# Optimization experiments

Measured on AMD Instinct MI355X. Metric: run time of the kernel, lower is better.

Reference implementation:

```python
import jax, jax.numpy as jnp
import numpy as np

E = 256
H = 8
DH = E // H
N = 200000
NEG = -1e9


def _normalize(x, eps=1e-12):
    # torch F.normalize: x / max(||x||_2, eps) along last dim
    n = jnp.linalg.norm(x, axis=-1, keepdims=True)
    return x / jnp.maximum(n, eps)


def setup_inputs() -> dict:
    key = jax.random.key(0)
    ks = jax.random.split(key, 16)
    s = 1.0 / np.sqrt(E)
    inp = {
        "context_vector": jax.random.normal(ks[0], (3 * E,), jnp.float32),
        "node_embeddings": jax.random.normal(ks[1], (N, E), jnp.float32),
        "invalid_action_mask": jax.random.randint(ks[2], (N,), 0, 2).astype(bool),
        # project_context: Linear(3E, E)
        "Wc": jax.random.normal(ks[3], (E, 3 * E), jnp.float32) * (1.0 / np.sqrt(3 * E)),
        "bc": jnp.zeros((E,), jnp.float32),
        # project_keys / project_values: Linear(E, E)
        "Wk": jax.random.normal(ks[4], (E, E), jnp.float32) * s,
        "bk": jnp.zeros((E,), jnp.float32),
        "Wv": jax.random.normal(ks[5], (E, E), jnp.float32) * s,
        "bv": jnp.zeros((E,), jnp.float32),
        # nn.MultiheadAttention packed in-projection and out-projection
        "in_proj_w": jax.random.normal(ks[6], (3 * E, E), jnp.float32) * s,
        "in_proj_b": jnp.zeros((3 * E,), jnp.float32),
        "out_proj_w": jax.random.normal(ks[7], (E, E), jnp.float32) * s,
        "out_proj_b": jnp.zeros((E,), jnp.float32),
        # project_attn_output: Linear(E, E)
        "Wo": jax.random.normal(ks[8], (E, E), jnp.float32) * s,
        "bo": jnp.zeros((E,), jnp.float32),
    }
    # guarantee at least one valid action
    inp["invalid_action_mask"] = inp["invalid_action_mask"].at[0].set(False)
    return inp


def reference(context_vector, node_embeddings, invalid_action_mask,
              Wc, bc, Wk, bk, Wv, bv,
              in_proj_w, in_proj_b, out_proj_w, out_proj_b, Wo, bo):
    valid = ~invalid_action_mask                        # [N]

    query = context_vector @ Wc.T + bc                  # [E]
    keys = _normalize(node_embeddings @ Wk.T + bk)      # [N, E]
    values = _normalize(node_embeddings @ Wv.T + bv)    # [N, E]

    # MultiheadAttention, single query, batch 1
    wq, wk2, wv2 = in_proj_w[:E], in_proj_w[E:2 * E], in_proj_w[2 * E:]
    bq, bk2, bv2 = in_proj_b[:E], in_proj_b[E:2 * E], in_proj_b[2 * E:]
    q = (query @ wq.T + bq).reshape(H, DH)              # [H, DH]
    k = (keys @ wk2.T + bk2).reshape(N, H, DH)          # [N, H, DH]
    v = (values @ wv2.T + bv2).reshape(N, H, DH)

    logits = jnp.einsum("hd,nhd->hn", q, k) / np.sqrt(DH)   # [H, N]
    logits = jnp.where(valid[None, :], logits, NEG)
    w = jax.nn.softmax(logits, axis=-1)                 # [H, N]
    attn = jnp.einsum("hn,nhd->hd", w, v).reshape(E)    # [E]
    attn = attn @ out_proj_w.T + out_proj_b             # [E]

    attn = _normalize(attn @ Wo.T + bo)                 # [E]

    # pointer scores over valid nodes (invalid -> prob 0)
    scores = jnp.where(valid, keys @ attn, NEG)         # [N]
    probs = jax.nn.softmax(scores)                      # [N]
    return probs
```

## Files before the change

kernel.cpp:

```cpp
#include <hip/hip_runtime.h>

#define NN 200000
#define NEGV -1000000000.0f

typedef __attribute__((ext_vector_type(8))) short bf16x8;
typedef __attribute__((ext_vector_type(4))) float f32x4;
typedef __attribute__((ext_vector_type(4))) unsigned int u32x4;

__device__ __forceinline__ float bf2f(unsigned short u){
  unsigned int x = ((unsigned int)u) << 16;
  return __builtin_bit_cast(float, x);
}
__device__ __forceinline__ unsigned short f2bf(float f){
  unsigned int x = __builtin_bit_cast(unsigned int, f);
  x += 0x7fffu + ((x >> 16) & 1u);
  return (unsigned short)(x >> 16);
}

static constexpr size_t OFF_RK     = 0;
static constexpr size_t OFF_RV     = 800256;
static constexpr size_t OFF_LOGITS = 1600512;
static constexpr size_t OFF_SCORES = 8000512;
static constexpr size_t OFF_QUERY  = 8800768;
static constexpr size_t OFF_Q2     = 8801792;
static constexpr size_t OFF_A2     = 8802816;
static constexpr size_t OFF_CONSTS = 8811008;
static constexpr size_t OFF_BIMG   = 8811264;
static constexpr size_t OFF_LSTAT  = 9081600;
static constexpr size_t OFF_MZ     = 9089792;
static constexpr size_t OFF_KATTN  = 9089856;
static constexpr size_t OFF_KB     = 9090880;
static constexpr size_t OFF_UPART  = 9090944;
static constexpr size_t OFF_TPART  = 13285248;
static constexpr size_t OFF_U      = 13301632;
static constexpr size_t OFF_T      = 13309824;
static constexpr size_t OFF_P3STAT = 13309888;
static constexpr size_t OFF_MZ3    = 13313984;
static constexpr size_t OFF_EMBBF  = 13314048;
static constexpr size_t WS_NEED_BF = OFF_EMBBF + (size_t)NN*512;

__global__ void k_prep1(const float* __restrict__ ctx, const float* __restrict__ Wc,
                        const float* __restrict__ bc, float* __restrict__ query){
  int tid = threadIdx.x, lane = tid & 63, wave = tid >> 6;
  float4 c0 = *(const float4*)(ctx + lane*4);
  float4 c1 = *(const float4*)(ctx + 256 + lane*4);
  float4 c2 = *(const float4*)(ctx + 512 + lane*4);
  #pragma unroll
  for (int rr = 0; rr < 2; rr++){
    int r = blockIdx.x*8 + wave*2 + rr;
    float4 w0 = *(const float4*)(Wc + (size_t)r*768 + lane*4);
    float4 w1 = *(const float4*)(Wc + (size_t)r*768 + 256 + lane*4);
    float4 w2 = *(const float4*)(Wc + (size_t)r*768 + 512 + lane*4);
    float d = w0.x*c0.x + w0.y*c0.y + w0.z*c0.z + w0.w*c0.w
            + w1.x*c1.x + w1.y*c1.y + w1.z*c1.z + w1.w*c1.w
            + w2.x*c2.x + w2.y*c2.y + w2.z*c2.z + w2.w*c2.w;
    #pragma unroll
    for (int m = 1; m < 64; m <<= 1) d += __shfl_xor(d, m);
    if (lane == 0) query[r] = d + bc[r];
  }
}

__global__ void k_prep2(const float* __restrict__ ipw, const float* __restrict__ ipb,
                        const float* __restrict__ query, float* __restrict__ q2){
  int tid = threadIdx.x, lane = tid & 63, wave = tid >> 6;
  float4 x4 = *(const float4*)(query + lane*4);
  #pragma unroll
  for (int rr = 0; rr < 2; rr++){
    int r = blockIdx.x*8 + wave*2 + rr;
    float4 w4 = *(const float4*)(ipw + (size_t)r*256 + lane*4);
    float d = w4.x*x4.x + w4.y*x4.y + w4.z*x4.z + w4.w*x4.w;
    #pragma unroll
    for (int m = 1; m < 64; m <<= 1) d += __shfl_xor(d, m);
    if (lane == 0) q2[r] = d + ipb[r];
  }
}

__global__ void k_prep3(const float* __restrict__ ipw, const float* __restrict__ ipb,
                        const float* __restrict__ q2, float* __restrict__ AH,
                        float* __restrict__ consts){
  int h = blockIdx.x, t = threadIdx.x;
  __shared__ float qs[32];
  if (t < 32) qs[t] = q2[h*32 + t];
  __syncthreads();
  float a = 0.f;
  #pragma unroll
  for (int d = 0; d < 32; d++) a += qs[d] * ipw[(size_t)(256 + h*32 + d)*256 + t];
  AH[h*256 + t] = a;
  if (t == 0){
    float ck = 0.f;
    for (int d = 0; d < 32; d++) ck += qs[d] * ipb[256 + h*32 + d];
    consts[8 + h] = ck;
  }
}

__global__ void k_prep4(const float* __restrict__ Wk, const float* __restrict__ AH,
                        float* __restrict__ A2p){
  int b = blockIdx.x, h = b >> 3, seg = b & 7, t = threadIdx.x;
  __shared__ float as[32];
  if (t < 32) as[t] = AH[h*256 + seg*32 + t];
  __syncthreads();
  float acc = 0.f;
  #pragma unroll
  for (int i = 0; i < 32; i++) acc += as[i] * Wk[(size_t)(seg*32 + i)*256 + t];
  A2p[(size_t)b*256 + t] = acc;
}

__global__ void k_prep5(const float* __restrict__ A2p, const float* __restrict__ AH,
                        const float* __restrict__ bk, float* __restrict__ A2,
                        float* __restrict__ consts){
  int h = blockIdx.x, t = threadIdx.x, lane = t & 63, wave = t >> 6;
  float s = 0.f;
  #pragma unroll
  for (int seg = 0; seg < 8; seg++) s += A2p[(size_t)(h*8 + seg)*256 + t];
  A2[h*256 + t] = s;
  float cc = AH[h*256 + t] * bk[t];
  #pragma unroll
  for (int m = 1; m < 64; m <<= 1) cc += __shfl_xor(cc, m);
  __shared__ float red[4];
  if (lane == 0) red[wave] = cc;
  __syncthreads();
  if (t == 0) consts[h] = red[0] + red[1] + red[2] + red[3];
}

__global__ void k_bimg(const float* __restrict__ Wk, const float* __restrict__ Wv,
                       const float* __restrict__ A2, unsigned char* __restrict__ bimg){
  int g = blockIdx.x*256 + threadIdx.x;
  if (g >= 8*528*4) return;
  int s = g / (528*4);
  int rem = g % (528*4);
  int col = rem >> 2, kg = rem & 3;
  int j0 = s*32 + kg*8;
  const float* src = nullptr;
  if (col < 256) src = Wk + col*256 + j0;
  else if (col < 512) src = Wv + (col-256)*256 + j0;
  else if (col < 520) src = A2 + (col-512)*256 + j0;
  unsigned short u[8];
  #pragma unroll
  for (int i = 0; i < 8; i++) u[i] = src ? f2bf(src[i]) : (unsigned short)0;
  uint4 o;
  o.x = (unsigned int)u[0] | ((unsigned int)u[1] << 16);
  o.y = (unsigned int)u[2] | ((unsigned int)u[3] << 16);
  o.z = (unsigned int)u[4] | ((unsigned int)u[5] << 16);
  o.w = (unsigned int)u[6] | ((unsigned int)u[7] << 16);
  unsigned int addr = (unsigned int)((col*64 + kg*16) ^ ((col & 7) << 4));
  *(uint4*)(bimg + (size_t)s*33792 + addr) = o;
}

__launch_bounds__(512)
__global__ void k_main(const float* __restrict__ emb, const unsigned char* __restrict__ bimg,
                       const int* __restrict__ mask, const float* __restrict__ consts,
                       float* __restrict__ rk_g, float* __restrict__ rv_g,
                       float* __restrict__ logits, unsigned char* __restrict__ ebf){
  __shared__ float part[4][4][16];
  __shared__ float rkbuf[64];
  const int tid = threadIdx.x;
  const int lane = tid & 63, wave = tid >> 6;
  const int sp = wave >> 2, ch = wave & 3;
  const int c = lane & 15, kg = lane >> 4;
  const int nb0 = blockIdx.x * 64;
  const unsigned bOff = (unsigned)((c*64 + kg*16) ^ ((c & 7) << 4));
  const int node0 = (sp*2 + 0)*16 + c;
  const int node1 = (sp*2 + 1)*16 + c;
  const bool wr = (ch == 0) && (ebf != nullptr);

  f32x4 acc[2][9];
  #pragma unroll
  for (int st = 0; st < 2; st++)
    #pragma unroll
    for (int f = 0; f < 9; f++) acc[st][f] = (f32x4){0.f, 0.f, 0.f, 0.f};

  #pragma unroll 2
  for (int s = 0; s < 8; s++){
    const float* a0p = emb + (size_t)(nb0 + node0)*256 + s*32 + kg*8;
    const float* a1p = emb + (size_t)(nb0 + node1)*256 + s*32 + kg*8;
    float4 x0 = *(const float4*)a0p, x1 = *(const float4*)(a0p + 4);
    float4 y0 = *(const float4*)a1p, y1 = *(const float4*)(a1p + 4);
    u32x4 u0, u1;
    u0.x = (unsigned int)f2bf(x0.x) | ((unsigned int)f2bf(x0.y) << 16);
    u0.y = (unsigned int)f2bf(x0.z) | ((unsigned int)f2bf(x0.w) << 16);
    u0.z = (unsigned int)f2bf(x1.x) | ((unsigned int)f2bf(x1.y) << 16);
    u0.w = (unsigned int)f2bf(x1.z) | ((unsigned int)f2bf(x1.w) << 16);
    u1.x = (unsigned int)f2bf(y0.x) | ((unsigned int)f2bf(y0.y) << 16);
    u1.y = (unsigned int)f2bf(y0.z) | ((unsigned int)f2bf(y0.w) << 16);
    u1.z = (unsigned int)f2bf(y1.x) | ((unsigned int)f2bf(y1.y) << 16);
    u1.w = (unsigned int)f2bf(y1.z) | ((unsigned int)f2bf(y1.w) << 16);
    bf16x8 af0 = __builtin_bit_cast(bf16x8, u0);
    bf16x8 af1 = __builtin_bit_cast(bf16x8, u1);
    if (wr){
      unsigned char* base = ebf + (size_t)blockIdx.x*32768 + (size_t)s*4096;
      __builtin_nontemporal_store(u0, (u32x4*)(base + node0*64 + kg*16));
      __builtin_nontemporal_store(u1, (u32x4*)(base + node1*64 + kg*16));
    }
    const unsigned char* bs = bimg + (size_t)s*33792;
    #pragma unroll
    for (int f = 0; f < 9; f++){
      int cf = (f < 8) ? (ch*8 + f) : 32;
      bf16x8 bfv = *(const bf16x8*)(bs + (size_t)cf*1024 + bOff);
      acc[0][f] = __builtin_amdgcn_mfma_f32_16x16x32_bf16(af0, bfv, acc[0][f], 0, 0, 0);
      acc[1][f] = __builtin_amdgcn_mfma_f32_16x16x32_bf16(af1, bfv, acc[1][f], 0, 0, 0);
    }
  }

  #pragma unroll
  for (int st = 0; st < 2; st++){
    #pragma unroll
    for (int i = 0; i < 4; i++){
      float pp = 0.f;
      #pragma unroll
      for (int f = 0; f < 8; f++) pp += acc[st][f][i]*acc[st][f][i];
      #pragma unroll
      for (int m = 1; m < 16; m <<= 1) pp += __shfl_xor(pp, m);
      if (c == 0) part[ch][2*sp + st][kg*4 + i] = pp;
    }
  }
  __syncthreads();
  if (tid < 64){
    int gs = tid >> 4, r = tid & 15;
    float rk = fmaxf(sqrtf(part[0][gs][r] + part[1][gs][r]), 1e-12f);
    float rv = fmaxf(sqrtf(part[2][gs][r] + part[3][gs][r]), 1e-12f);
    rk_g[nb0 + tid] = rk; rv_g[nb0 + tid] = rv;
    rkbuf[tid] = rk;
  }
  __syncthreads();
  if (ch == 3 && c < 8){
    const float rs32 = 0.17677669529663688f;
    float cb = consts[c], ck = consts[8 + c];
    #pragma unroll
    for (int st = 0; st < 2; st++){
      #pragma unroll
      for (int i = 0; i < 4; i++){
        int nl = (2*sp + st)*16 + kg*4 + i;
        int n = nb0 + nl;
        float lg = (mask[n] == 0) ? ((acc[st][8][i] + cb)*rs32/rkbuf[nl] + ck*rs32) : NEGV;
        logits[(size_t)n*8 + c] = lg;
      }
    }
  }
}

__global__ void k_lstats(const float* __restrict__ logits, float* __restrict__ lstat){
  int tid = threadIdx.x;
  float m[8], z[8];
  #pragma unroll
  for (int h = 0; h < 8; h++){ m[h] = -3.0e38f; z[h] = 0.f; }
  for (int n = blockIdx.x*256 + tid; n < NN; n += 128*256){
    float4 a = *(const float4*)(logits + (size_t)n*8);
    float4 b = *(const float4*)(logits + (size_t)n*8 + 4);
    float l[8] = {a.x,a.y,a.z,a.w,b.x,b.y,b.z,b.w};
    #pragma unroll
    for (int h = 0; h < 8; h++){
      float M = fmaxf(m[h], l[h]);
      z[h] = z[h]*expf(m[h]-M) + expf(l[h]-M);
      m[h] = M;
    }
  }
  #pragma unroll
  for (int s = 1; s < 64; s <<= 1){
    #pragma unroll
    for (int h = 0; h < 8; h++){
      float m2 = __shfl_xor(m[h], s), z2 = __shfl_xor(z[h], s);
      float M = fmaxf(m[h], m2);
      z[h] = z[h]*expf(m[h]-M) + z2*expf(m2-M);
      m[h] = M;
    }
  }
  __shared__ float sm[4][8], sz[4][8];
  int wave = tid >> 6, lane = tid & 63;
  if (lane == 0){
    #pragma unroll
    for (int h = 0; h < 8; h++){ sm[wave][h] = m[h]; sz[wave][h] = z[h]; }
  }
  __syncthreads();
  if (tid < 8){
    float M = sm[0][tid], Z = sz[0][tid];
    #pragma unroll
    for (int w = 1; w < 4; w++){
      float M2 = fmaxf(M, sm[w][tid]);
      Z = Z*expf(M-M2) + sz[w][tid]*expf(sm[w][tid]-M2);
      M = M2;
    }
    lstat[(blockIdx.x*8 + tid)*2] = M;
    lstat[(blockIdx.x*8 + tid)*2 + 1] = Z;
  }
}

__global__ void k_mz(const float* __restrict__ lstat, float* __restrict__ MZ){
  int t = threadIdx.x;
  int h = t >> 3, seg = t & 7;
  float m = -3.0e38f, z = 0.f;
  for (int k = 0; k < 16; k++){
    int b = seg*16 + k;
    float m2 = lstat[(b*8 + h)*2], z2 = lstat[(b*8 + h)*2 + 1];
    float M = fmaxf(m, m2); z = z*expf(m-M) + z2*expf(m2-M); m = M;
  }
  #pragma unroll
  for (int s = 1; s < 8; s <<= 1){
    float m2 = __shfl_xor(m, s), z2 = __shfl_xor(z, s);
    float M = fmaxf(m, m2); z = z*expf(m-M) + z2*expf(m2-M); m = M;
  }
  if (seg == 0){ MZ[h] = m; MZ[8+h] = z; }
}

template<int BF>
__launch_bounds__(256)
__global__ void k_wsum(const void* __restrict__ embsrc, const float* __restrict__ logits,
                       const float* __restrict__ rv_g, const float* __restrict__ MZ,
                       float* __restrict__ upart, float* __restrict__ tpart){
  int tid = threadIdx.x, lane = tid & 63, wave = tid >> 6;
  int hl = lane & 31, h2 = lane >> 5;
  int gw = blockIdx.x*4 + wave;
  float Mh = MZ[hl & 7];
  float ua[8][8];
  #pragma unroll
  for (int h = 0; h < 8; h++)
    #pragma unroll
    for (int j = 0; j < 8; j++) ua[h][j] = 0.f;
  float tacc = 0.f;
  for (int p = gw; p < NN/2; p += 2048){
    int n = 2*p + h2;
    float e[8];
    if (BF){
      size_t addr = (size_t)(n >> 6)*32768 + (size_t)(hl >> 2)*4096
                  + (size_t)(n & 63)*64 + (size_t)(hl & 3)*16;
      uint4 g = *(const uint4*)((const unsigned char*)embsrc + addr);
      e[0]=bf2f((unsigned short)(g.x&0xffff)); e[1]=bf2f((unsigned short)(g.x>>16));
      e[2]=bf2f((unsigned short)(g.y&0xffff)); e[3]=bf2f((unsigned short)(g.y>>16));
      e[4]=bf2f((unsigned short)(g.z&0xffff)); e[5]=bf2f((unsigned short)(g.z>>16));
      e[6]=bf2f((unsigned short)(g.w&0xffff)); e[7]=bf2f((unsigned short)(g.w>>16));
    } else {
      const float* ep = (const float*)embsrc + (size_t)n*256 + hl*8;
      float4 a = *(const float4*)ep, b = *(const float4*)(ep + 4);
      e[0]=a.x; e[1]=a.y; e[2]=a.z; e[3]=a.w; e[4]=b.x; e[5]=b.y; e[6]=b.z; e[7]=b.w;
    }
    float coef = 0.f;
    if (hl < 8) coef = expf(logits[(size_t)n*8 + hl] - Mh) / rv_g[n];
    tacc += coef;
    #pragma unroll
    for (int h = 0; h < 8; h++){
      float ch = __shfl(coef, h, 32);
      #pragma unroll
      for (int j = 0; j < 8; j++) ua[h][j] += ch * e[j];
    }
  }
  #pragma unroll
  for (int h = 0; h < 8; h++)
    #pragma unroll
    for (int j = 0; j < 8; j++) ua[h][j] += __shfl_xor(ua[h][j], 32);
  tacc += __shfl_xor(tacc, 32);
  __shared__ float ub[4][8][256];
  __shared__ float tb[4][8];
  if (h2 == 0){
    #pragma unroll
    for (int h = 0; h < 8; h++)
      #pragma unroll
      for (int j = 0; j < 8; j++) ub[wave][h][hl*8 + j] = ua[h][j];
    if (hl < 8) tb[wave][hl] = tacc;
  }
  __syncthreads();
  #pragma unroll
  for (int rep = 0; rep < 8; rep++){
    int idx = rep*256 + tid;
    int h = idx >> 8, j = idx & 255;
    upart[(size_t)blockIdx.x*2048 + h*256 + j] = ub[0][h][j]+ub[1][h][j]+ub[2][h][j]+ub[3][h][j];
  }
  if (tid < 8) tpart[blockIdx.x*8 + tid] = tb[0][tid]+tb[1][tid]+tb[2][tid]+tb[3][tid];
}

__global__ void k_ured(const float* __restrict__ upart, const float* __restrict__ tpart,
                       float* __restrict__ U, float* __restrict__ T){
  int b = blockIdx.x; int h = b >> 3, js = b & 7;
  int t = threadIdx.x; int j = js*32 + (t & 31); int br = t >> 5;
  float s = 0.f;
  for (int k = 0; k < 64; k++){
    int bb = k*8 + br;
    s += upart[(size_t)bb*2048 + h*256 + j];
  }
  __shared__ float sb[8][32];
  sb[br][t & 31] = s;
  __syncthreads();
  if (t < 32){
    float tot = 0.f;
    #pragma unroll
    for (int r = 0; r < 8; r++) tot += sb[r][t];
    U[h*256 + js*32 + t] = tot;
  }
  if (js == 0){
    float tp = 0.f;
    for (int i = t; i < 512; i += 256) tp += tpart[i*8 + h];
    #pragma unroll
    for (int m = 1; m < 64; m <<= 1) tp += __shfl_xor(tp, m);
    __shared__ float rr[4];
    if ((t & 63) == 0) rr[t >> 6] = tp;
    __syncthreads();
    if (t == 0) T[h] = rr[0]+rr[1]+rr[2]+rr[3];
  }
}

__global__ void k_att1(const float* __restrict__ U, const float* __restrict__ T,
                       const float* __restrict__ MZ, const float* __restrict__ Wv,
                       const float* __restrict__ bv, float* __restrict__ sh2g){
  int tid = threadIdx.x, lane = tid & 63, wave = tid >> 6;
  float4 uh[8];
  #pragma unroll
  for (int h = 0; h < 8; h++) uh[h] = *(const float4*)(U + h*256 + lane*4);
  #pragma unroll
  for (int rr = 0; rr < 2; rr++){
    int r = blockIdx.x*8 + wave*2 + rr;
    float4 w4 = *(const float4*)(Wv + (size_t)r*256 + lane*4);
    float acc[8];
    #pragma unroll
    for (int h = 0; h < 8; h++)
      acc[h] = w4.x*uh[h].x + w4.y*uh[h].y + w4.z*uh[h].z + w4.w*uh[h].w;
    #pragma unroll
    for (int m = 1; m < 64; m <<= 1)
      #pragma unroll
      for (int h = 0; h < 8; h++) acc[h] += __shfl_xor(acc[h], m);
    if (lane == 0){
      float bvr = bv[r];
      #pragma unroll
      for (int h = 0; h < 8; h++) sh2g[h*256 + r] = (acc[h] + bvr*T[h]) / MZ[8+h];
    }
  }
}

__global__ void k_att2(const float* __restrict__ ipw, const float* __restrict__ ipb,
                       const float* __restrict__ sh2g, float* __restrict__ a1g){
  int tid = threadIdx.x, lane = tid & 63, wave = tid >> 6;
  #pragma unroll
  for (int rr = 0; rr < 2; rr++){
    int r = blockIdx.x*8 + wave*2 + rr;
    int h = r >> 5;
    float4 x4 = *(const float4*)(sh2g + h*256 + lane*4);
    float4 w4 = *(const float4*)(ipw + (size_t)(512 + r)*256 + lane*4);
    float d = w4.x*x4.x + w4.y*x4.y + w4.z*x4.z + w4.w*x4.w;
    #pragma unroll
    for (int m = 1; m < 64; m <<= 1) d += __shfl_xor(d, m);
    if (lane == 0) a1g[r] = d + ipb[512 + r];
  }
}

__global__ void k_matvec(const float* __restrict__ W, const float* __restrict__ b,
                         const float* __restrict__ x, float* __restrict__ y){
  int tid = threadIdx.x, lane = tid & 63, wave = tid >> 6;
  float4 x4 = *(const float4*)(x + lane*4);
  #pragma unroll
  for (int rr = 0; rr < 2; rr++){
    int r = blockIdx.x*8 + wave*2 + rr;
    float4 w4 = *(const float4*)(W + (size_t)r*256 + lane*4);
    float d = w4.x*x4.x + w4.y*x4.y + w4.z*x4.z + w4.w*x4.w;
    #pragma unroll
    for (int m = 1; m < 64; m <<= 1) d += __shfl_xor(d, m);
    if (lane == 0) y[r] = d + b[r];
  }
}

__global__ void k_att5(const float* __restrict__ Wk, const float* __restrict__ o2g,
                       float* __restrict__ kp){
  int b = blockIdx.x, t = threadIdx.x;
  __shared__ float os[32];
  if (t < 32) os[t] = o2g[b*32 + t];
  __syncthreads();
  float acc = 0.f;
  #pragma unroll
  for (int i = 0; i < 32; i++) acc += os[i] * Wk[(size_t)(b*32 + i)*256 + t];
  kp[b*256 + t] = acc;
}

__global__ void k_fin(const float* __restrict__ o2g, const float* __restrict__ kp,
                      const float* __restrict__ bk, float* __restrict__ kattn,
                      float* __restrict__ kbout){
  int t = threadIdx.x, lane = t & 63, wave = t >> 6;
  __shared__ float red[4], red2[4];
  float o2v = o2g[t];
  float sq = o2v*o2v;
  #pragma unroll
  for (int m = 1; m < 64; m <<= 1) sq += __shfl_xor(sq, m);
  if (lane == 0) red[wave] = sq;
  float cb = o2v * bk[t];
  #pragma unroll
  for (int m = 1; m < 64; m <<= 1) cb += __shfl_xor(cb, m);
  if (lane == 0) red2[wave] = cb;
  __syncthreads();
  float nrm = fmaxf(sqrtf(red[0]+red[1]+red[2]+red[3]), 1e-12f);
  float s = 0.f;
  #pragma unroll
  for (int b = 0; b < 8; b++) s += kp[b*256 + t];
  kattn[t] = s / nrm;
  if (t == 0) kbout[0] = (red2[0]+red2[1]+red2[2]+red2[3]) / nrm;
}

template<int BF>
__launch_bounds__(256)
__global__ void k_scores(const void* __restrict__ embsrc, const float* __restrict__ rk_g,
                         const int* __restrict__ mask, const float* __restrict__ kattn,
                         const float* __restrict__ kbp, float* __restrict__ scores,
                         float* __restrict__ p3stat){
  int tid = threadIdx.x, lane = tid & 63, wave = tid >> 6;
  int hl = lane & 31, h2 = lane >> 5;
  __shared__ float ka[256];
  ka[tid] = kattn[tid];
  __syncthreads();
  float kb = kbp[0];
  float kv[8];
  #pragma unroll
  for (int j = 0; j < 8; j++) kv[j] = ka[hl*8 + j];
  int gw = blockIdx.x*4 + wave;
  float m = -3.0e38f, z = 0.f;
  for (int p = gw; p < NN/2; p += 2048){
    int n = 2*p + h2;
    float d;
    if (BF){
      size_t addr = (size_t)(n >> 6)*32768 + (size_t)(hl >> 2)*4096
                  + (size_t)(n & 63)*64 + (size_t)(hl & 3)*16;
      uint4 g = *(const uint4*)((const unsigned char*)embsrc + addr);
      d  = bf2f((unsigned short)(g.x&0xffff))*kv[0] + bf2f((unsigned short)(g.x>>16))*kv[1];
      d += bf2f((unsigned short)(g.y&0xffff))*kv[2] + bf2f((unsigned short)(g.y>>16))*kv[3];
      d += bf2f((unsigned short)(g.z&0xffff))*kv[4] + bf2f((unsigned short)(g.z>>16))*kv[5];
      d += bf2f((unsigned short)(g.w&0xffff))*kv[6] + bf2f((unsigned short)(g.w>>16))*kv[7];
    } else {
      const float* ep = (const float*)embsrc + (size_t)n*256 + hl*8;
      float4 a = *(const float4*)ep, b = *(const float4*)(ep + 4);
      d = a.x*kv[0]+a.y*kv[1]+a.z*kv[2]+a.w*kv[3]+b.x*kv[4]+b.y*kv[5]+b.z*kv[6]+b.w*kv[7];
    }
    #pragma unroll
    for (int s = 1; s < 32; s <<= 1) d += __shfl_xor(d, s);
    if (hl == 0){
      float sc = (mask[n] == 0) ? ((d + kb) / rk_g[n]) : NEGV;
      scores[n] = sc;
      float M = fmaxf(m, sc);
      z = z*expf(m - M) + expf(sc - M);
      m = M;
    }
  }
  float m2 = __shfl_xor(m, 32), z2 = __shfl_xor(z, 32);
  float M = fmaxf(m, m2); z = z*expf(m-M) + z2*expf(m2-M); m = M;
  __shared__ float rm[4], rz[4];
  if (lane == 0){ rm[wave] = m; rz[wave] = z; }
  __syncthreads();
  if (tid == 0){
    float Mx = rm[0], Z = rz[0];
    for (int w = 1; w < 4; w++){
      float M2 = fmaxf(Mx, rm[w]);
      Z = Z*expf(Mx - M2) + rz[w]*expf(rm[w] - M2);
      Mx = M2;
    }
    p3stat[blockIdx.x*2] = Mx; p3stat[blockIdx.x*2+1] = Z;
  }
}

__global__ void k_mz3(const float* __restrict__ p3stat, float* __restrict__ MZ3){
  int t = threadIdx.x;
  float m = p3stat[t*2], z = p3stat[t*2+1];
  {
    float m2 = p3stat[(t+256)*2], z2 = p3stat[(t+256)*2+1];
    float M = fmaxf(m, m2); z = z*expf(m-M) + z2*expf(m2-M); m = M;
  }
  #pragma unroll
  for (int mm = 1; mm < 64; mm <<= 1){
    float ms = __shfl_xor(m, mm), zs = __shfl_xor(z, mm);
    float Mx = fmaxf(m, ms); z = z*expf(m-Mx) + zs*expf(ms-Mx); m = Mx;
  }
  __shared__ float rm[4], rz[4];
  if ((t&63)==0){ rm[t>>6]=m; rz[t>>6]=z; }
  __syncthreads();
  if (t==0){
    float M=rm[0], Z=rz[0];
    for (int w=1; w<4; w++){ float Mx=fmaxf(M,rm[w]); Z=Z*expf(M-Mx)+rz[w]*expf(rm[w]-Mx); M=Mx; }
    MZ3[0]=M; MZ3[1]=Z;
  }
}

__global__ void k_probs(const float* __restrict__ scores, const float* __restrict__ MZ3,
                        float* __restrict__ out){
  float M = MZ3[0], iZ = 1.0f / MZ3[1];
  for (int n = blockIdx.x*256 + threadIdx.x; n < NN; n += 512*256)
    out[n] = expf(scores[n] - M) * iZ;
}

extern "C" void kernel_launch(void* const* d_in, const int* in_sizes, int n_in,
                              void* d_out, int out_size, void* d_ws, size_t ws_size,
                              hipStream_t stream){
  (void)in_sizes; (void)n_in; (void)out_size;
  const float* ctx = (const float*)d_in[0];
  const float* emb = (const float*)d_in[1];
  const int*   mask= (const int*)d_in[2];
  const float* Wc  = (const float*)d_in[3];
  const float* bc  = (const float*)d_in[4];
  const float* Wk  = (const float*)d_in[5];
  const float* bk  = (const float*)d_in[6];
  const float* Wv  = (const float*)d_in[7];
  const float* bv  = (const float*)d_in[8];
  const float* ipw = (const float*)d_in[9];
  const float* ipb = (const float*)d_in[10];
  const float* opw = (const float*)d_in[11];
  const float* opb = (const float*)d_in[12];
  const float* Wo  = (const float*)d_in[13];
  const float* bo  = (const float*)d_in[14];
  float* out = (float*)d_out;
  char* ws = (char*)d_ws;

  float* rk     = (float*)(ws + OFF_RK);
  float* rv     = (float*)(ws + OFF_RV);
  float* logits = (float*)(ws + OFF_LOGITS);
  float* scores = (float*)(ws + OFF_SCORES);
  float* query  = (float*)(ws + OFF_QUERY);
  float* q2     = (float*)(ws + OFF_Q2);
  float* A2     = (float*)(ws + OFF_A2);
  float* consts = (float*)(ws + OFF_CONSTS);
  unsigned char* bimg = (unsigned char*)(ws + OFF_BIMG);
  float* lstat  = (float*)(ws + OFF_LSTAT);
  float* MZ     = (float*)(ws + OFF_MZ);
  float* kattn  = (float*)(ws + OFF_KATTN);
  float* kb     = (float*)(ws + OFF_KB);
  float* upart  = (float*)(ws + OFF_UPART);
  float* tpart  = (float*)(ws + OFF_TPART);
  float* U      = (float*)(ws + OFF_U);
  float* T      = (float*)(ws + OFF_T);
  float* p3stat = (float*)(ws + OFF_P3STAT);
  float* MZ3    = (float*)(ws + OFF_MZ3);
  float* AH   = (float*)(ws + OFF_UPART + 32768);
  float* A2p  = (float*)(ws + OFF_UPART + 65536);
  float* sh2g = (float*)(ws + OFF_UPART + 0);
  float* a1g  = (float*)(ws + OFF_UPART + 8192);
  float* o1g  = (float*)(ws + OFF_UPART + 9216);
  float* o2g  = (float*)(ws + OFF_UPART + 10240);
  float* kp   = (float*)(ws + OFF_UPART + 11264);

  const bool bf = ws_size >= WS_NEED_BF;
  unsigned char* ebf = bf ? (unsigned char*)(ws + OFF_EMBBF) : nullptr;

  k_prep1 <<<32,  256, 0, stream>>>(ctx, Wc, bc, query);
  k_prep2 <<<32,  256, 0, stream>>>(ipw, ipb, query, q2);
  k_prep3 <<<8,   256, 0, stream>>>(ipw, ipb, q2, AH, consts);
  k_prep4 <<<64,  256, 0, stream>>>(Wk, AH, A2p);
  k_prep5 <<<8,   256, 0, stream>>>(A2p, AH, bk, A2, consts);
  k_bimg  <<<66,  256, 0, stream>>>(Wk, Wv, A2, bimg);
  k_main  <<<3125,512, 0, stream>>>(emb, bimg, mask, consts, rk, rv, logits, ebf);
  k_lstats<<<128, 256, 0, stream>>>(logits, lstat);
  k_mz    <<<1,   64,  0, stream>>>(lstat, MZ);
  if (bf) k_wsum<1><<<512, 256, 0, stream>>>(ebf, logits, rv, MZ, upart, tpart);
  else    k_wsum<0><<<512, 256, 0, stream>>>(emb, logits, rv, MZ, upart, tpart);
  k_ured  <<<64,  256, 0, stream>>>(upart, tpart, U, T);
  k_att1  <<<32,  256, 0, stream>>>(U, T, MZ, Wv, bv, sh2g);
  k_att2  <<<32,  256, 0, stream>>>(ipw, ipb, sh2g, a1g);
  k_matvec<<<32,  256, 0, stream>>>(opw, opb, a1g, o1g);
  k_matvec<<<32,  256, 0, stream>>>(Wo, bo, o1g, o2g);
  k_att5  <<<8,   256, 0, stream>>>(Wk, o2g, kp);
  k_fin   <<<1,   256, 0, stream>>>(o2g, kp, bk, kattn, kb);
  if (bf) k_scores<1><<<512, 256, 0, stream>>>(ebf, rk, mask, kattn, kb, scores, p3stat);
  else    k_scores<0><<<512, 256, 0, stream>>>(emb, rk, mask, kattn, kb, scores, p3stat);
  k_mz3   <<<1,   256, 0, stream>>>(p3stat, MZ3);
  k_probs <<<512, 256, 0, stream>>>(scores, MZ3, out);
}
```

Measured before the change: 377.1 us.

## Split bf16 conversion into a standalone pass and feed k_main from bf16 copy

Adds a separate streaming kernel that converts the fp32 embeddings to a row-major bf16 copy. k_main then reads bf16 directly with software-prefetched register buffers, using 256-thread blocks over 32 nodes instead of 512 threads over 64. The bf16 layout changes from blocked to plain row-major, so k_wsum and k_scores index it more simply. This moves the conversion out of the MFMA loop and lets it run as a pure bandwidth pass, at the cost of one extra full read of the fp32 embeddings and a re-read of the bf16 copy in k_main.

```diff
diff --git a/kernel.cpp b/kernel.cpp
--- a/kernel.cpp
+++ b/kernel.cpp
@@ -39,6 +39,21 @@
 static constexpr size_t OFF_EMBBF  = 13314048;
 static constexpr size_t WS_NEED_BF = OFF_EMBBF + (size_t)NN*512;
 
+__global__ void k_conv(const float* __restrict__ emb, unsigned char* __restrict__ ebf){
+  size_t stride = (size_t)gridDim.x * blockDim.x;
+  for (size_t g = (size_t)blockIdx.x*blockDim.x + threadIdx.x; g < (size_t)NN*32; g += stride){
+    const float* src = emb + g*8;
+    float4 a = *(const float4*)src;
+    float4 b = *(const float4*)(src + 4);
+    u32x4 o;
+    o.x = (unsigned int)f2bf(a.x) | ((unsigned int)f2bf(a.y) << 16);
+    o.y = (unsigned int)f2bf(a.z) | ((unsigned int)f2bf(a.w) << 16);
+    o.z = (unsigned int)f2bf(b.x) | ((unsigned int)f2bf(b.y) << 16);
+    o.w = (unsigned int)f2bf(b.z) | ((unsigned int)f2bf(b.w) << 16);
+    *(u32x4*)(ebf + g*16) = o;
+  }
+}
+
 __global__ void k_prep1(const float* __restrict__ ctx, const float* __restrict__ Wc,
                         const float* __restrict__ bc, float* __restrict__ query){
   int tid = threadIdx.x, lane = tid & 63, wave = tid >> 6;
@@ -146,22 +161,20 @@
   *(uint4*)(bimg + (size_t)s*33792 + addr) = o;
 }
 
-__launch_bounds__(512)
-__global__ void k_main(const float* __restrict__ emb, const unsigned char* __restrict__ bimg,
+template<int BF>
+__launch_bounds__(256)
+__global__ void k_main(const float* __restrict__ emb, const unsigned char* __restrict__ ebf,
+                       const unsigned char* __restrict__ bimg,
                        const int* __restrict__ mask, const float* __restrict__ consts,
                        float* __restrict__ rk_g, float* __restrict__ rv_g,
-                       float* __restrict__ logits, unsigned char* __restrict__ ebf){
-  __shared__ float part[4][4][16];
-  __shared__ float rkbuf[64];
+                       float* __restrict__ logits){
+  __shared__ float part[4][2][16];
+  __shared__ float rkbuf[32];
   const int tid = threadIdx.x;
-  const int lane = tid & 63, wave = tid >> 6;
-  const int sp = wave >> 2, ch = wave & 3;
+  const int lane = tid & 63, ch = tid >> 6;
   const int c = lane & 15, kg = lane >> 4;
-  const int nb0 = blockIdx.x * 64;
+  const int nb0 = blockIdx.x * 32;
   const unsigned bOff = (unsigned)((c*64 + kg*16) ^ ((c & 7) << 4));
-  const int node0 = (sp*2 + 0)*16 + c;
-  const int node1 = (sp*2 + 1)*16 + c;
-  const bool wr = (ch == 0) && (ebf != nullptr);
 
   f32x4 acc[2][9];
   #pragma unroll
@@ -169,35 +182,55 @@
     #pragma unroll
     for (int f = 0; f < 9; f++) acc[st][f] = (f32x4){0.f, 0.f, 0.f, 0.f};
 
-  #pragma unroll 2
-  for (int s = 0; s < 8; s++){
-    const float* a0p = emb + (size_t)(nb0 + node0)*256 + s*32 + kg*8;
-    const float* a1p = emb + (size_t)(nb0 + node1)*256 + s*32 + kg*8;
-    float4 x0 = *(const float4*)a0p, x1 = *(const float4*)(a0p + 4);
-    float4 y0 = *(const float4*)a1p, y1 = *(const float4*)(a1p + 4);
-    u32x4 u0, u1;
-    u0.x = (unsigned int)f2bf(x0.x) | ((unsigned int)f2bf(x0.y) << 16);
-    u0.y = (unsigned int)f2bf(x0.z) | ((unsigned int)f2bf(x0.w) << 16);
-    u0.z = (unsigned int)f2bf(x1.x) | ((unsigned int)f2bf(x1.y) << 16);
-    u0.w = (unsigned int)f2bf(x1.z) | ((unsigned int)f2bf(x1.w) << 16);
-    u1.x = (unsigned int)f2bf(y0.x) | ((unsigned int)f2bf(y0.y) << 16);
-    u1.y = (unsigned int)f2bf(y0.z) | ((unsigned int)f2bf(y0.w) << 16);
-    u1.z = (unsigned int)f2bf(y1.x) | ((unsigned int)f2bf(y1.y) << 16);
-    u1.w = (unsigned int)f2bf(y1.z) | ((unsigned int)f2bf(y1.w) << 16);
-    bf16x8 af0 = __builtin_bit_cast(bf16x8, u0);
-    bf16x8 af1 = __builtin_bit_cast(bf16x8, u1);
-    if (wr){
-      unsigned char* base = ebf + (size_t)blockIdx.x*32768 + (size_t)s*4096;
-      __builtin_nontemporal_store(u0, (u32x4*)(base + node0*64 + kg*16));
-      __builtin_nontemporal_store(u1, (u32x4*)(base + node1*64 + kg*16));
-    }
-    const unsigned char* bs = bimg + (size_t)s*33792;
-    #pragma unroll
-    for (int f = 0; f < 9; f++){
-      int cf = (f < 8) ? (ch*8 + f) : 32;
-      bf16x8 bfv = *(const bf16x8*)(bs + (size_t)cf*1024 + bOff);
-      acc[0][f] = __builtin_amdgcn_mfma_f32_16x16x32_bf16(af0, bfv, acc[0][f], 0, 0, 0);
-      acc[1][f] = __builtin_amdgcn_mfma_f32_16x16x32_bf16(af1, bfv, acc[1][f], 0, 0, 0);
+  if (BF){
+    const unsigned char* aB0 = ebf + (size_t)(nb0 + c)*512 + kg*16;
+    const unsigned char* aB1 = ebf + (size_t)(nb0 + 16 + c)*512 + kg*16;
+    bf16x8 pa0[8], pa1[8];
+    pa0[0] = *(const bf16x8*)(aB0);
+    pa1[0] = *(const bf16x8*)(aB1);
+    pa0[1] = *(const bf16x8*)(aB0 + 64);
+    pa1[1] = *(const bf16x8*)(aB1 + 64);
+    #pragma unroll
+    for (int s = 0; s < 8; s++){
+      if (s < 6){
+        pa0[s+2] = *(const bf16x8*)(aB0 + (s+2)*64);
+        pa1[s+2] = *(const bf16x8*)(aB1 + (s+2)*64);
+      }
+      const unsigned char* bs = bimg + (size_t)s*33792 + bOff;
+      #pragma unroll
+      for (int f = 0; f < 9; f++){
+        const int cf = (f < 8) ? (ch*8 + f) : 32;
+        bf16x8 bfv = *(const bf16x8*)(bs + (size_t)cf*1024);
+        acc[0][f] = __builtin_amdgcn_mfma_f32_16x16x32_bf16(pa0[s], bfv, acc[0][f], 0, 0, 0);
+        acc[1][f] = __builtin_amdgcn_mfma_f32_16x16x32_bf16(pa1[s], bfv, acc[1][f], 0, 0, 0);
+      }
+    }
+  } else {
+    #pragma unroll 2
+    for (int s = 0; s < 8; s++){
+      const float* a0p = emb + (size_t)(nb0 + c)*256 + s*32 + kg*8;
+      const float* a1p = emb + (size_t)(nb0 + 16 + c)*256 + s*32 + kg*8;
+      float4 x0 = *(const float4*)a0p, x1 = *(const float4*)(a0p + 4);
+      float4 y0 = *(const float4*)a1p, y1 = *(const float4*)(a1p + 4);
+      u32x4 u0, u1;
+      u0.x = (unsigned int)f2bf(x0.x) | ((unsigned int)f2bf(x0.y) << 16);
+      u0.y = (unsigned int)f2bf(x0.z) | ((unsigned int)f2bf(x0.w) << 16);
+      u0.z = (unsigned int)f2bf(x1.x) | ((unsigned int)f2bf(x1.y) << 16);
+      u0.w = (unsigned int)f2bf(x1.z) | ((unsigned int)f2bf(x1.w) << 16);
+      u1.x = (unsigned int)f2bf(y0.x) | ((unsigned int)f2bf(y0.y) << 16);
+      u1.y = (unsigned int)f2bf(y0.z) | ((unsigned int)f2bf(y0.w) << 16);
+      u1.z = (unsigned int)f2bf(y1.x) | ((unsigned int)f2bf(y1.y) << 16);
+      u1.w = (unsigned int)f2bf(y1.z) | ((unsigned int)f2bf(y1.w) << 16);
+      bf16x8 af0 = __builtin_bit_cast(bf16x8, u0);
+      bf16x8 af1 = __builtin_bit_cast(bf16x8, u1);
+      const unsigned char* bs = bimg + (size_t)s*33792 + bOff;
+      #pragma unroll
+      for (int f = 0; f < 9; f++){
+        const int cf = (f < 8) ? (ch*8 + f) : 32;
+        bf16x8 bfv = *(const bf16x8*)(bs + (size_t)cf*1024);
+        acc[0][f] = __builtin_amdgcn_mfma_f32_16x16x32_bf16(af0, bfv, acc[0][f], 0, 0, 0);
+        acc[1][f] = __builtin_amdgcn_mfma_f32_16x16x32_bf16(af1, bfv, acc[1][f], 0, 0, 0);
+      }
     }
   }
 
@@ -210,11 +243,11 @@
       for (int f = 0; f < 8; f++) pp += acc[st][f][i]*acc[st][f][i];
       #pragma unroll
       for (int m = 1; m < 16; m <<= 1) pp += __shfl_xor(pp, m);
-      if (c == 0) part[ch][2*sp + st][kg*4 + i] = pp;
-    }
-  }
-  __syncthreads();
-  if (tid < 64){
+      if (c == 0) part[ch][st][kg*4 + i] = pp;
+    }
+  }
+  __syncthreads();
+  if (tid < 32){
     int gs = tid >> 4, r = tid & 15;
     float rk = fmaxf(sqrtf(part[0][gs][r] + part[1][gs][r]), 1e-12f);
     float rv = fmaxf(sqrtf(part[2][gs][r] + part[3][gs][r]), 1e-12f);
@@ -229,7 +262,7 @@
     for (int st = 0; st < 2; st++){
       #pragma unroll
       for (int i = 0; i < 4; i++){
-        int nl = (2*sp + st)*16 + kg*4 + i;
+        int nl = st*16 + kg*4 + i;
         int n = nb0 + nl;
         float lg = (mask[n] == 0) ? ((acc[st][8][i] + cb)*rs32/rkbuf[nl] + ck*rs32) : NEGV;
         logits[(size_t)n*8 + c] = lg;
@@ -320,9 +353,7 @@
     int n = 2*p + h2;
     float e[8];
     if (BF){
-      size_t addr = (size_t)(n >> 6)*32768 + (size_t)(hl >> 2)*4096
-                  + (size_t)(n & 63)*64 + (size_t)(hl & 3)*16;
-      uint4 g = *(const uint4*)((const unsigned char*)embsrc + addr);
+      uint4 g = *(const uint4*)((const unsigned char*)embsrc + (size_t)n*512 + hl*16);
       e[0]=bf2f((unsigned short)(g.x&0xffff)); e[1]=bf2f((unsigned short)(g.x>>16));
       e[2]=bf2f((unsigned short)(g.y&0xffff)); e[3]=bf2f((unsigned short)(g.y>>16));
       e[4]=bf2f((unsigned short)(g.z&0xffff)); e[5]=bf2f((unsigned short)(g.z>>16));
@@ -510,9 +541,7 @@
     int n = 2*p + h2;
     float d;
     if (BF){
-      size_t addr = (size_t)(n >> 6)*32768 + (size_t)(hl >> 2)*4096
-                  + (size_t)(n & 63)*64 + (size_t)(hl & 3)*16;
-      uint4 g = *(const uint4*)((const unsigned char*)embsrc + addr);
+      uint4 g = *(const uint4*)((const unsigned char*)embsrc + (size_t)n*512 + hl*16);
       d  = bf2f((unsigned short)(g.x&0xffff))*kv[0] + bf2f((unsigned short)(g.x>>16))*kv[1];
       d += bf2f((unsigned short)(g.y&0xffff))*kv[2] + bf2f((unsigned short)(g.y>>16))*kv[3];
       d += bf2f((unsigned short)(g.z&0xffff))*kv[4] + bf2f((unsigned short)(g.z>>16))*kv[5];
@@ -629,13 +658,15 @@
   const bool bf = ws_size >= WS_NEED_BF;
   unsigned char* ebf = bf ? (unsigned char*)(ws + OFF_EMBBF) : nullptr;
 
+  if (bf) k_conv<<<2048, 256, 0, stream>>>(emb, ebf);
   k_prep1 <<<32,  256, 0, stream>>>(ctx, Wc, bc, query);
   k_prep2 <<<32,  256, 0, stream>>>(ipw, ipb, query, q2);
   k_prep3 <<<8,   256, 0, stream>>>(ipw, ipb, q2, AH, consts);
   k_prep4 <<<64,  256, 0, stream>>>(Wk, AH, A2p);
   k_prep5 <<<8,   256, 0, stream>>>(A2p, AH, bk, A2, consts);
   k_bimg  <<<66,  256, 0, stream>>>(Wk, Wv, A2, bimg);
-  k_main  <<<3125,512, 0, stream>>>(emb, bimg, mask, consts, rk, rv, logits, ebf);
+  if (bf) k_main<1><<<6250, 256, 0, stream>>>(emb, ebf, bimg, mask, consts, rk, rv, logits);
+  else    k_main<0><<<6250, 256, 0, stream>>>(emb, nullptr, bimg, mask, consts, rk, rv, logits);
   k_lstats<<<128, 256, 0, stream>>>(logits, lstat);
   k_mz    <<<1,   64,  0, stream>>>(lstat, MZ);
   if (bf) k_wsum<1><<<512, 256, 0, stream>>>(ebf, logits, rv, MZ, upart, tpart);
```

Measured after the change: 324.7 us. 1.16x faster.
